# Kernel tuning notes

Hardware: AMD Instinct MI355X
Metric: run time of the kernel (lower is better)

Reference implementation:

```python
import jax, jax.numpy as jnp
import numpy as np

N_NODES = 50000
N_EDGES = 800000
IN_DIM = 128
H = 8
D = 16  # per-head out_dim; H*D == 128
CLAMP = 5.0


def setup_inputs() -> dict:
    key = jax.random.key(0)
    ks = jax.random.split(key, 9)
    xavier = lambda k, shape: jax.random.normal(k, shape, dtype=jnp.float32) * np.sqrt(2.0 / (shape[0] + shape[1]))
    x = jax.random.normal(ks[0], (N_NODES, IN_DIM), dtype=jnp.float32)
    edge_attr = jax.random.normal(ks[1], (N_EDGES, IN_DIM), dtype=jnp.float32)
    edge_index = jax.random.randint(ks[2], (2, N_EDGES), 0, N_NODES)
    WQ = xavier(ks[3], (IN_DIM, H * D))
    bQ = jnp.zeros((H * D,), dtype=jnp.float32)
    WK = xavier(ks[4], (IN_DIM, H * D))
    WV = xavier(ks[5], (IN_DIM, H * D))
    WE1 = xavier(ks[6], (IN_DIM, H * D))
    bE1 = jnp.zeros((H * D,), dtype=jnp.float32)
    return {"x": x, "edge_attr": edge_attr, "edge_index": edge_index,
            "WQ": WQ, "bQ": bQ, "WK": WK, "WV": WV, "WE1": WE1, "bE1": bE1}


def reference(x, edge_attr, edge_index, WQ, bQ, WK, WV, WE1, bE1):
    N = x.shape[0]
    src, dst = edge_index[0], edge_index[1]
    # projections (K/V have no bias: use_bias=False)
    Q = (x @ WQ + bQ).reshape(N, H, D)
    K = (x @ WK).reshape(N, H, D)
    V = (x @ WV).reshape(N, H, D)
    E = (edge_attr @ WE1 + bE1).reshape(-1, H, D)  # [Ne,H,D]
    # edge-gather elementwise QK product conditioned on E (attn_product='mul')
    score_e = K[src] * Q[dst] * E                  # [Ne,H,D]
    wE = score_e.reshape(score_e.shape[0], -1)     # [Ne,H*D]
    # scalar per-edge-per-head score (attn_reweight=False -> sum over D)
    score_h = score_e.sum(-1, keepdims=True) / jnp.sqrt(jnp.float32(D))
    score_h = jnp.clip(score_h, -CLAMP, CLAMP)     # [Ne,H,1]
    # pyg_softmax: segment-wise softmax keyed on destination node
    seg_max = jax.ops.segment_max(score_h, dst, num_segments=N)
    ex = jnp.exp(score_h - seg_max[dst])
    denom = jax.ops.segment_sum(ex, dst, num_segments=N)[dst] + 1e-16
    alpha = ex / denom                             # [Ne,H,1]
    # scatter-add aggregation of weighted values
    wV = jax.ops.segment_sum(V[src] * alpha, dst, num_segments=N)
    # edge enhance (edge_reweight=False -> rowV = score_e)
    wV = wV + jax.ops.segment_sum(score_e * alpha, dst, num_segments=N)
    return wV, wE
```

## Files before the change

kernel.cpp:

```cpp
#include <hip/hip_runtime.h>
#include <hip/hip_bf16.h>

#define NNODES 50000
#define NEDGES 800000
#define NHEAD 8

typedef __attribute__((ext_vector_type(8))) short short8v;
typedef __attribute__((ext_vector_type(4))) float f32x4;

union U8 { short8v v; unsigned short u[8]; };

__device__ inline unsigned short f2bf(float f) {
    unsigned int u = __float_as_uint(f);
    unsigned int r = (u + 0x7FFFu + ((u >> 16) & 1u)) >> 16;
    return (unsigned short)r;
}
__device__ inline float bf2f(unsigned int u) {
    return __uint_as_float(u << 16);
}

__global__ void prep_weights(const float* __restrict__ WQ, const float* __restrict__ WK,
                             const float* __restrict__ WV, const float* __restrict__ WE1,
                             unsigned short* __restrict__ Wt) {
    int idx = blockIdx.x * 256 + threadIdx.x;
    if (idx >= 4 * 16384) return;
    int m = idx >> 14, r = idx & 16383;
    int k = r >> 7, n = r & 127;
    const float* W = (m == 0) ? WQ : (m == 1) ? WK : (m == 2) ? WV : WE1;
    Wt[m * 16384 + n * 128 + k] = f2bf(W[k * 128 + n]);
}

__device__ inline int swz(int row, int byteInRow) {
    return row * 256 + (byteInRow ^ ((row & 15) << 4));
}

__device__ inline void stageW256(char* Wl, const unsigned short* __restrict__ Wtm, int t) {
    int row = t >> 1, half = t & 1;
    const unsigned short* src = Wtm + row * 128 + half * 64;
#pragma unroll
    for (int i = 0; i < 8; i++) {
        short8v v = *reinterpret_cast<const short8v*>(src + i * 8);
        *reinterpret_cast<short8v*>(Wl + swz(row, half * 128 + i * 16)) = v;
    }
}

__device__ inline void stageW512(char* Wl, const unsigned short* __restrict__ Wtm, int t) {
    int row = t >> 2, q = t & 3;
    const unsigned short* src = Wtm + row * 128 + q * 32;
#pragma unroll
    for (int i = 0; i < 4; i++) {
        short8v v = *reinterpret_cast<const short8v*>(src + i * 8);
        *reinterpret_cast<short8v*>(Wl + swz(row, q * 64 + i * 16)) = v;
    }
}

__device__ inline void loadAfrag(const float* aptr, int lg, short8v* a, bool ok) {
#pragma unroll
    for (int kk = 0; kk < 4; kk++) {
        U8 h;
        if (ok) {
            float4 f0 = *reinterpret_cast<const float4*>(aptr + kk * 32 + lg * 8);
            float4 f1 = *reinterpret_cast<const float4*>(aptr + kk * 32 + lg * 8 + 4);
            h.u[0] = f2bf(f0.x); h.u[1] = f2bf(f0.y); h.u[2] = f2bf(f0.z); h.u[3] = f2bf(f0.w);
            h.u[4] = f2bf(f1.x); h.u[5] = f2bf(f1.y); h.u[6] = f2bf(f1.z); h.u[7] = f2bf(f1.w);
        } else {
#pragma unroll
            for (int j = 0; j < 8; j++) h.u[j] = 0;
        }
        a[kk] = h.v;
    }
}

__global__ __launch_bounds__(256, 4) void proj_qkv(const float* __restrict__ x,
                                                   const unsigned short* __restrict__ Wt,
                                                   const float* __restrict__ bQ,
                                                   float* __restrict__ Q, float* __restrict__ K,
                                                   float* __restrict__ V) {
    __shared__ __align__(16) char Wl[32768];
    int t = threadIdx.x;
    int nb = blockIdx.x * 64;
    int lane = t & 63, w = t >> 6;
    int lg = lane >> 4, lr = lane & 15;

    int arow = nb + w * 16 + lr;
    bool ok = arow < NNODES;
    short8v a[4];
    loadAfrag(x + (size_t)arow * 128, lg, a, ok);

    float bq[8];
#pragma unroll
    for (int n = 0; n < 8; n++) bq[n] = bQ[n * 16 + lr];

    for (int m = 0; m < 3; m++) {
        __syncthreads();
        stageW256(Wl, Wt + m * 16384, t);
        __syncthreads();

        f32x4 acc[8];
#pragma unroll
        for (int n = 0; n < 8; n++) acc[n] = (f32x4){0.f, 0.f, 0.f, 0.f};
#pragma unroll
        for (int kk = 0; kk < 4; kk++) {
#pragma unroll
            for (int n = 0; n < 8; n++) {
                short8v b = *reinterpret_cast<short8v*>(Wl + swz(n * 16 + lr, (kk * 32 + lg * 8) * 2));
                acc[n] = __builtin_amdgcn_mfma_f32_16x16x32_bf16(a[kk], b, acc[n], 0, 0, 0);
            }
        }
        float* out = (m == 0) ? Q : (m == 1) ? K : V;
#pragma unroll
        for (int n = 0; n < 8; n++) {
            int c = n * 16 + lr;
            float bias = (m == 0) ? bq[n] : 0.f;
#pragma unroll
            for (int r = 0; r < 4; r++) {
                int gr = nb + w * 16 + lg * 4 + r;
                if (gr < NNODES) out[(size_t)gr * 128 + c] = acc[n][r] + bias;
            }
        }
    }
}

__global__ __launch_bounds__(512, 6) void edge_score(const float* __restrict__ EA,
                                                     const unsigned short* __restrict__ Wt,
                                                     const float* __restrict__ bE1,
                                                     const int* __restrict__ eidx,
                                                     const float* __restrict__ Q,
                                                     const float* __restrict__ K,
                                                     float* __restrict__ wE,
                                                     float* __restrict__ scoreH,
                                                     float* __restrict__ denom) {
    __shared__ __align__(16) char Wl[32768];
    __shared__ int srcL[128], dstL[128];
    int t = threadIdx.x;
    int eb = blockIdx.x * 128;
    int lane = t & 63, w = t >> 6;
    int lg = lane >> 4, lr = lane & 15;

    stageW512(Wl, Wt + 3 * 16384, t);
    if (t < 128) srcL[t] = eidx[eb + t];
    else if (t < 256) dstL[t - 128] = eidx[NEDGES + eb + t - 128];
    float be[8];
#pragma unroll
    for (int n = 0; n < 8; n++) be[n] = bE1[n * 16 + lr];

    int arow = eb + w * 16 + lr;
    short8v a[4];
    loadAfrag(EA + (size_t)arow * 128, lg, a, true);

    __syncthreads();

    f32x4 acc[8];
#pragma unroll
    for (int n = 0; n < 8; n++) acc[n] = (f32x4){0.f, 0.f, 0.f, 0.f};
#pragma unroll
    for (int kk = 0; kk < 4; kk++) {
#pragma unroll
        for (int n = 0; n < 8; n++) {
            short8v b = *reinterpret_cast<short8v*>(Wl + swz(n * 16 + lr, (kk * 32 + lg * 8) * 2));
            acc[n] = __builtin_amdgcn_mfma_f32_16x16x32_bf16(a[kk], b, acc[n], 0, 0, 0);
        }
    }

    __syncthreads();

#pragma unroll
    for (int n = 0; n < 8; n++) {
#pragma unroll
        for (int r = 0; r < 4; r++) {
            int row = w * 16 + lg * 4 + r;
            *reinterpret_cast<unsigned short*>(Wl + swz(row, (n * 16 + lr) * 2)) =
                f2bf(acc[n][r] + be[n]);
        }
    }

    int h = lane >> 3;
#pragma unroll 4
    for (int i = 0; i < 16; i++) {
        int loc = w * 16 + i;
        int e = eb + loc;
        int s = srcL[loc], d = dstL[loc];
        unsigned int ep = *reinterpret_cast<unsigned int*>(Wl + swz(loc, lane * 4));
        float e0 = bf2f(ep & 0xffffu);
        float e1 = bf2f(ep >> 16);
        float2 kv = *reinterpret_cast<const float2*>(K + (size_t)s * 128 + lane * 2);
        float2 qv = *reinterpret_cast<const float2*>(Q + (size_t)d * 128 + lane * 2);
        float s0 = e0 * kv.x * qv.x;
        float s1 = e1 * kv.y * qv.y;
        *reinterpret_cast<float2*>(wE + (size_t)e * 128 + lane * 2) = make_float2(s0, s1);
        float sum = s0 + s1;
        sum += __shfl_xor(sum, 1);
        sum += __shfl_xor(sum, 2);
        sum += __shfl_xor(sum, 4);
        if ((lane & 7) == 0) {
            float sh = fminf(fmaxf(sum * 0.25f, -5.f), 5.f);
            float ex = __expf(sh);
            scoreH[(size_t)e * 8 + h] = ex;
            unsafeAtomicAdd(&denom[d * 8 + h], ex);
        }
    }
}

__global__ void hist_kernel(const int* __restrict__ eidx, int* __restrict__ histo) {
    int e = blockIdx.x * 256 + threadIdx.x;
    if (e >= NEDGES) return;
    atomicAdd(&histo[eidx[NEDGES + e]], 1);
}

__global__ __launch_bounds__(256) void scanA(const int* __restrict__ histo, int* __restrict__ bsum) {
    __shared__ int l[4];
    int t = threadIdx.x;
    int idx = blockIdx.x * 256 + t;
    int v = (idx < NNODES) ? histo[idx] : 0;
#pragma unroll
    for (int off = 32; off; off >>= 1) v += __shfl_down(v, off);
    if ((t & 63) == 0) l[t >> 6] = v;
    __syncthreads();
    if (t == 0) bsum[blockIdx.x] = l[0] + l[1] + l[2] + l[3];
}

__global__ __launch_bounds__(256) void scanB(const int* __restrict__ bsum, int* __restrict__ boff) {
    __shared__ int l[256];
    int t = threadIdx.x;
    int v = (t < 196) ? bsum[t] : 0;
    l[t] = v;
    __syncthreads();
    for (int off = 1; off < 256; off <<= 1) {
        int tmp = (t >= off) ? l[t - off] : 0;
        __syncthreads();
        l[t] += tmp;
        __syncthreads();
    }
    if (t < 196) boff[t] = l[t] - v;
}

__global__ __launch_bounds__(256) void scanC(const int* __restrict__ histo,
                                             const int* __restrict__ boff,
                                             int* __restrict__ start, int* __restrict__ cursor) {
    __shared__ int l[256];
    int t = threadIdx.x;
    int idx = blockIdx.x * 256 + t;
    int v = (idx < NNODES) ? histo[idx] : 0;
    l[t] = v;
    __syncthreads();
    for (int off = 1; off < 256; off <<= 1) {
        int tmp = (t >= off) ? l[t - off] : 0;
        __syncthreads();
        l[t] += tmp;
        __syncthreads();
    }
    int excl = l[t] - v + boff[blockIdx.x];
    if (idx <= NNODES) {
        start[idx] = excl;
        if (idx < NNODES) cursor[idx] = excl;
    }
}

__global__ void scatter_edges(const int* __restrict__ eidx, int* __restrict__ cursor,
                              int* __restrict__ sortedE) {
    int e = blockIdx.x * 256 + threadIdx.x;
    if (e >= NEDGES) return;
    int d = eidx[NEDGES + e];
    int pos = atomicAdd(&cursor[d], 1);
    sortedE[pos] = e;
}

__global__ __launch_bounds__(256) void aggregate_pernode(const int* __restrict__ sortedE,
                                                         const int* __restrict__ start,
                                                         const int* __restrict__ eidx,
                                                         const float* __restrict__ scoreH,
                                                         const float* __restrict__ denom,
                                                         const float* __restrict__ V,
                                                         const float* __restrict__ wE,
                                                         float* __restrict__ wV) {
    __shared__ int eL[4][64];
    __shared__ int sL[4][64];
    __shared__ float aL[4][512];
    int w = threadIdx.x >> 6;
    int n = blockIdx.x * 4 + w;
    if (n >= NNODES) return;
    int lane = threadIdx.x & 63;
    int half = lane >> 5, li = lane & 31;
    int col = li * 4, h = li >> 2;
    int s0 = start[n], cnt = start[n + 1] - s0;

    float4 d0 = *reinterpret_cast<const float4*>(denom + n * 8);
    float4 d1 = *reinterpret_cast<const float4*>(denom + n * 8 + 4);
    float inv[8];
    inv[0] = 1.f / (d0.x + 1e-16f); inv[1] = 1.f / (d0.y + 1e-16f);
    inv[2] = 1.f / (d0.z + 1e-16f); inv[3] = 1.f / (d0.w + 1e-16f);
    inv[4] = 1.f / (d1.x + 1e-16f); inv[5] = 1.f / (d1.y + 1e-16f);
    inv[6] = 1.f / (d1.z + 1e-16f); inv[7] = 1.f / (d1.w + 1e-16f);

    float4 ac = make_float4(0.f, 0.f, 0.f, 0.f);

    for (int cb = 0; cb < cnt; cb += 64) {
        int ccnt = min(64, cnt - cb);
        int e = 0, s = 0;
        float4 p0 = make_float4(0.f, 0.f, 0.f, 0.f), p1 = p0;
        if (lane < ccnt) {
            e = sortedE[s0 + cb + lane];
            s = eidx[e];
            p0 = *reinterpret_cast<const float4*>(scoreH + (size_t)e * 8);
            p1 = *reinterpret_cast<const float4*>(scoreH + (size_t)e * 8 + 4);
        }
        eL[w][lane] = e;
        sL[w][lane] = s;
        aL[w][lane * 8 + 0] = p0.x * inv[0]; aL[w][lane * 8 + 1] = p0.y * inv[1];
        aL[w][lane * 8 + 2] = p0.z * inv[2]; aL[w][lane * 8 + 3] = p0.w * inv[3];
        aL[w][lane * 8 + 4] = p1.x * inv[4]; aL[w][lane * 8 + 5] = p1.y * inv[5];
        aL[w][lane * 8 + 6] = p1.z * inv[6]; aL[w][lane * 8 + 7] = p1.w * inv[7];
        asm volatile("s_waitcnt lgkmcnt(0)" ::: "memory");
        __builtin_amdgcn_sched_barrier(0);
        int np = (ccnt + 1) >> 1;
#pragma unroll 2
        for (int i = 0; i < np; i++) {
            int ii = i * 2 + half;
            int e2 = eL[w][ii], s2 = sL[w][ii];
            float al = aL[w][ii * 8 + h];
            float4 we = *reinterpret_cast<const float4*>(wE + (size_t)e2 * 128 + col);
            float4 vv = *reinterpret_cast<const float4*>(V + (size_t)s2 * 128 + col);
            ac.x += (vv.x + we.x) * al;
            ac.y += (vv.y + we.y) * al;
            ac.z += (vv.z + we.z) * al;
            ac.w += (vv.w + we.w) * al;
        }
    }
    ac.x += __shfl_xor(ac.x, 32);
    ac.y += __shfl_xor(ac.y, 32);
    ac.z += __shfl_xor(ac.z, 32);
    ac.w += __shfl_xor(ac.w, 32);
    if (half == 0) *reinterpret_cast<float4*>(wV + (size_t)n * 128 + col) = ac;
}

extern "C" void kernel_launch(void* const* d_in, const int* in_sizes, int n_in,
                              void* d_out, int out_size, void* d_ws, size_t ws_size,
                              hipStream_t stream) {
    const float* x    = (const float*)d_in[0];
    const float* ea   = (const float*)d_in[1];
    const int*   eidx = (const int*)d_in[2];
    const float* WQ   = (const float*)d_in[3];
    const float* bQ   = (const float*)d_in[4];
    const float* WK   = (const float*)d_in[5];
    const float* WV   = (const float*)d_in[6];
    const float* WE1  = (const float*)d_in[7];
    const float* bE1  = (const float*)d_in[8];

    float* wV = (float*)d_out;
    float* wE = (float*)d_out + (size_t)NNODES * 128;

    float* Q      = (float*)d_ws;
    float* K      = Q + (size_t)NNODES * 128;
    float* V      = K + (size_t)NNODES * 128;
    float* scoreH = V + (size_t)NNODES * 128;
    float* denom  = scoreH + (size_t)NEDGES * 8;
    unsigned short* Wt = (unsigned short*)(denom + (size_t)NNODES * 8);
    int* histo   = (int*)(Wt + 4 * 16384);
    int* start   = histo + 50176;
    int* cursor  = start + 50177;
    int* sortedE = cursor + 50176;
    int* bsum    = sortedE + NEDGES;
    int* boff    = bsum + 256;

    hipMemsetAsync(histo, 0, (size_t)50176 * 4, stream);
    hipMemsetAsync(denom, 0, (size_t)NNODES * 8 * 4, stream);

    prep_weights<<<(4 * 16384 + 255) / 256, 256, 0, stream>>>(WQ, WK, WV, WE1, Wt);
    hist_kernel<<<(NEDGES + 255) / 256, 256, 0, stream>>>(eidx, histo);
    scanA<<<196, 256, 0, stream>>>(histo, bsum);
    scanB<<<1, 256, 0, stream>>>(bsum, boff);
    scanC<<<196, 256, 0, stream>>>(histo, boff, start, cursor);
    scatter_edges<<<(NEDGES + 255) / 256, 256, 0, stream>>>(eidx, cursor, sortedE);
    proj_qkv<<<(NNODES + 63) / 64, 256, 0, stream>>>(x, Wt, bQ, Q, K, V);
    edge_score<<<NEDGES / 128, 512, 0, stream>>>(ea, Wt, bE1, eidx, Q, K, wE, scoreH, denom);
    aggregate_pernode<<<(NNODES + 3) / 4, 256, 0, stream>>>(sortedE, start, eidx, scoreH, denom, V, wE, wV);
}
```

Baseline: 536.7 us.

## Fuse edge scoring and per-node aggregation into one destination-partitioned kernel

```diff
diff --git a/kernel.cpp b/kernel.cpp
--- a/kernel.cpp
+++ b/kernel.cpp
@@ -4,6 +4,9 @@
 #define NNODES 50000
 #define NEDGES 800000
 #define NHEAD 8
+#define CAP 96
+#define NBLK ((NEDGES + CAP - 1) / CAP)
+#define MAXSPAN 384
 
 typedef __attribute__((ext_vector_type(8))) short short8v;
 typedef __attribute__((ext_vector_type(4))) float f32x4;
@@ -121,86 +124,6 @@
     }
 }
 
-__global__ __launch_bounds__(512, 6) void edge_score(const float* __restrict__ EA,
-                                                     const unsigned short* __restrict__ Wt,
-                                                     const float* __restrict__ bE1,
-                                                     const int* __restrict__ eidx,
-                                                     const float* __restrict__ Q,
-                                                     const float* __restrict__ K,
-                                                     float* __restrict__ wE,
-                                                     float* __restrict__ scoreH,
-                                                     float* __restrict__ denom) {
-    __shared__ __align__(16) char Wl[32768];
-    __shared__ int srcL[128], dstL[128];
-    int t = threadIdx.x;
-    int eb = blockIdx.x * 128;
-    int lane = t & 63, w = t >> 6;
-    int lg = lane >> 4, lr = lane & 15;
-
-    stageW512(Wl, Wt + 3 * 16384, t);
-    if (t < 128) srcL[t] = eidx[eb + t];
-    else if (t < 256) dstL[t - 128] = eidx[NEDGES + eb + t - 128];
-    float be[8];
-#pragma unroll
-    for (int n = 0; n < 8; n++) be[n] = bE1[n * 16 + lr];
-
-    int arow = eb + w * 16 + lr;
-    short8v a[4];
-    loadAfrag(EA + (size_t)arow * 128, lg, a, true);
-
-    __syncthreads();
-
-    f32x4 acc[8];
-#pragma unroll
-    for (int n = 0; n < 8; n++) acc[n] = (f32x4){0.f, 0.f, 0.f, 0.f};
-#pragma unroll
-    for (int kk = 0; kk < 4; kk++) {
-#pragma unroll
-        for (int n = 0; n < 8; n++) {
-            short8v b = *reinterpret_cast<short8v*>(Wl + swz(n * 16 + lr, (kk * 32 + lg * 8) * 2));
-            acc[n] = __builtin_amdgcn_mfma_f32_16x16x32_bf16(a[kk], b, acc[n], 0, 0, 0);
-        }
-    }
-
-    __syncthreads();
-
-#pragma unroll
-    for (int n = 0; n < 8; n++) {
-#pragma unroll
-        for (int r = 0; r < 4; r++) {
-            int row = w * 16 + lg * 4 + r;
-            *reinterpret_cast<unsigned short*>(Wl + swz(row, (n * 16 + lr) * 2)) =
-                f2bf(acc[n][r] + be[n]);
-        }
-    }
-
-    int h = lane >> 3;
-#pragma unroll 4
-    for (int i = 0; i < 16; i++) {
-        int loc = w * 16 + i;
-        int e = eb + loc;
-        int s = srcL[loc], d = dstL[loc];
-        unsigned int ep = *reinterpret_cast<unsigned int*>(Wl + swz(loc, lane * 4));
-        float e0 = bf2f(ep & 0xffffu);
-        float e1 = bf2f(ep >> 16);
-        float2 kv = *reinterpret_cast<const float2*>(K + (size_t)s * 128 + lane * 2);
-        float2 qv = *reinterpret_cast<const float2*>(Q + (size_t)d * 128 + lane * 2);
-        float s0 = e0 * kv.x * qv.x;
-        float s1 = e1 * kv.y * qv.y;
-        *reinterpret_cast<float2*>(wE + (size_t)e * 128 + lane * 2) = make_float2(s0, s1);
-        float sum = s0 + s1;
-        sum += __shfl_xor(sum, 1);
-        sum += __shfl_xor(sum, 2);
-        sum += __shfl_xor(sum, 4);
-        if ((lane & 7) == 0) {
-            float sh = fminf(fmaxf(sum * 0.25f, -5.f), 5.f);
-            float ex = __expf(sh);
-            scoreH[(size_t)e * 8 + h] = ex;
-            unsafeAtomicAdd(&denom[d * 8 + h], ex);
-        }
-    }
-}
-
 __global__ void hist_kernel(const int* __restrict__ eidx, int* __restrict__ histo) {
     int e = blockIdx.x * 256 + threadIdx.x;
     if (e >= NEDGES) return;
@@ -265,59 +188,132 @@
     sortedE[pos] = e;
 }
 
-__global__ __launch_bounds__(256) void aggregate_pernode(const int* __restrict__ sortedE,
-                                                         const int* __restrict__ start,
-                                                         const int* __restrict__ eidx,
-                                                         const float* __restrict__ scoreH,
-                                                         const float* __restrict__ denom,
-                                                         const float* __restrict__ V,
-                                                         const float* __restrict__ wE,
-                                                         float* __restrict__ wV) {
-    __shared__ int eL[4][64];
-    __shared__ int sL[4][64];
-    __shared__ float aL[4][512];
-    int w = threadIdx.x >> 6;
-    int n = blockIdx.x * 4 + w;
-    if (n >= NNODES) return;
-    int lane = threadIdx.x & 63;
+__global__ void partition_blocks(const int* __restrict__ start, int* __restrict__ firstNode) {
+    int b = blockIdx.x * 256 + threadIdx.x;
+    if (b > NBLK) return;
+    int target = b * CAP;
+    int lo = 0, hi = NNODES;
+    while (lo < hi) {
+        int mid = (lo + hi) >> 1;
+        if (start[mid] < target) lo = mid + 1; else hi = mid;
+    }
+    firstNode[b] = lo;
+}
+
+__global__ __launch_bounds__(512, 6) void edge_mega(const float* __restrict__ EA,
+                                                    const unsigned short* __restrict__ Wt,
+                                                    const float* __restrict__ bE1,
+                                                    const int* __restrict__ eidx,
+                                                    const float* __restrict__ Q,
+                                                    const float* __restrict__ K,
+                                                    const float* __restrict__ V,
+                                                    const int* __restrict__ sortedE,
+                                                    const int* __restrict__ start,
+                                                    const int* __restrict__ firstNode,
+                                                    float* __restrict__ wE,
+                                                    float* __restrict__ wV) {
+    __shared__ __align__(16) char Wl[32768];
+    __shared__ float exL[MAXSPAN][8];
+    __shared__ int eG[MAXSPAN], sG[MAXSPAN], dG[MAXSPAN];
+
+    int b = blockIdx.x;
+    int n0 = firstNode[b], n1 = firstNode[b + 1];
+    if (n0 >= n1) return;
+    int gbase = start[n0];
+    int span = start[n1] - gbase;
+    if (span > MAXSPAN) span = MAXSPAN;
+
+    int t = threadIdx.x;
+    int lane = t & 63, w = t >> 6;
+    int lg = lane >> 4, lr = lane & 15;
+
+    for (int i = t; i < span; i += 512) {
+        int e = sortedE[gbase + i];
+        eG[i] = e;
+        sG[i] = eidx[e];
+        dG[i] = eidx[NEDGES + e];
+    }
+    __syncthreads();
+
+    float be[8];
+#pragma unroll
+    for (int n = 0; n < 8; n++) be[n] = bE1[n * 16 + lr];
+
+    for (int base = 0; base < span; base += 128) {
+        stageW512(Wl, Wt + 3 * 16384, t);
+
+        int slot = base + w * 16 + lr;
+        bool act = slot < span;
+        short8v a[4];
+        loadAfrag(EA + (size_t)(act ? eG[slot] : 0) * 128, lg, a, act);
+
+        __syncthreads();
+
+        f32x4 acc[8];
+#pragma unroll
+        for (int n = 0; n < 8; n++) acc[n] = (f32x4){0.f, 0.f, 0.f, 0.f};
+#pragma unroll
+        for (int kk = 0; kk < 4; kk++) {
+#pragma unroll
+            for (int n = 0; n < 8; n++) {
+                short8v bfr = *reinterpret_cast<short8v*>(Wl + swz(n * 16 + lr, (kk * 32 + lg * 8) * 2));
+                acc[n] = __builtin_amdgcn_mfma_f32_16x16x32_bf16(a[kk], bfr, acc[n], 0, 0, 0);
+            }
+        }
+        __syncthreads();
+
+#pragma unroll
+        for (int n = 0; n < 8; n++) {
+#pragma unroll
+            for (int r = 0; r < 4; r++) {
+                int row = w * 16 + lg * 4 + r;
+                *reinterpret_cast<unsigned short*>(Wl + swz(row, (n * 16 + lr) * 2)) =
+                    f2bf(acc[n][r] + be[n]);
+            }
+        }
+        int h = lane >> 3;
+#pragma unroll 4
+        for (int i = 0; i < 16; i++) {
+            int loc = w * 16 + i;
+            int slot2 = base + loc;
+            if (slot2 >= span) break;
+            int e = eG[slot2], s = sG[slot2], d = dG[slot2];
+            unsigned int ep = *reinterpret_cast<unsigned int*>(Wl + swz(loc, lane * 4));
+            float e0 = bf2f(ep & 0xffffu);
+            float e1 = bf2f(ep >> 16);
+            float2 kv = *reinterpret_cast<const float2*>(K + (size_t)s * 128 + lane * 2);
+            float2 qv = *reinterpret_cast<const float2*>(Q + (size_t)d * 128 + lane * 2);
+            float s0 = e0 * kv.x * qv.x;
+            float s1 = e1 * kv.y * qv.y;
+            *reinterpret_cast<float2*>(wE + (size_t)e * 128 + lane * 2) = make_float2(s0, s1);
+            float sum = s0 + s1;
+            sum += __shfl_xor(sum, 1);
+            sum += __shfl_xor(sum, 2);
+            sum += __shfl_xor(sum, 4);
+            if ((lane & 7) == 0) {
+                float sh = fminf(fmaxf(sum * 0.25f, -5.f), 5.f);
+                exL[slot2][h] = __expf(sh);
+            }
+        }
+        __syncthreads();
+    }
+
     int half = lane >> 5, li = lane & 31;
-    int col = li * 4, h = li >> 2;
-    int s0 = start[n], cnt = start[n + 1] - s0;
-
-    float4 d0 = *reinterpret_cast<const float4*>(denom + n * 8);
-    float4 d1 = *reinterpret_cast<const float4*>(denom + n * 8 + 4);
-    float inv[8];
-    inv[0] = 1.f / (d0.x + 1e-16f); inv[1] = 1.f / (d0.y + 1e-16f);
-    inv[2] = 1.f / (d0.z + 1e-16f); inv[3] = 1.f / (d0.w + 1e-16f);
-    inv[4] = 1.f / (d1.x + 1e-16f); inv[5] = 1.f / (d1.y + 1e-16f);
-    inv[6] = 1.f / (d1.z + 1e-16f); inv[7] = 1.f / (d1.w + 1e-16f);
-
-    float4 ac = make_float4(0.f, 0.f, 0.f, 0.f);
-
-    for (int cb = 0; cb < cnt; cb += 64) {
-        int ccnt = min(64, cnt - cb);
-        int e = 0, s = 0;
-        float4 p0 = make_float4(0.f, 0.f, 0.f, 0.f), p1 = p0;
-        if (lane < ccnt) {
-            e = sortedE[s0 + cb + lane];
-            s = eidx[e];
-            p0 = *reinterpret_cast<const float4*>(scoreH + (size_t)e * 8);
-            p1 = *reinterpret_cast<const float4*>(scoreH + (size_t)e * 8 + 4);
-        }
-        eL[w][lane] = e;
-        sL[w][lane] = s;
-        aL[w][lane * 8 + 0] = p0.x * inv[0]; aL[w][lane * 8 + 1] = p0.y * inv[1];
-        aL[w][lane * 8 + 2] = p0.z * inv[2]; aL[w][lane * 8 + 3] = p0.w * inv[3];
-        aL[w][lane * 8 + 4] = p1.x * inv[4]; aL[w][lane * 8 + 5] = p1.y * inv[5];
-        aL[w][lane * 8 + 6] = p1.z * inv[6]; aL[w][lane * 8 + 7] = p1.w * inv[7];
-        asm volatile("s_waitcnt lgkmcnt(0)" ::: "memory");
-        __builtin_amdgcn_sched_barrier(0);
-        int np = (ccnt + 1) >> 1;
-#pragma unroll 2
-        for (int i = 0; i < np; i++) {
-            int ii = i * 2 + half;
-            int e2 = eL[w][ii], s2 = sL[w][ii];
-            float al = aL[w][ii * 8 + h];
+    int col = li * 4, h2 = li >> 2;
+    int hh = lane >> 3, j = lane & 7;
+    for (int n = n0 + w; n < n1; n += 8) {
+        int sl0 = start[n] - gbase, sl1 = start[n + 1] - gbase;
+        float den = 0.f;
+        for (int ss = sl0 + j; ss < sl1; ss += 8) den += exL[ss][hh];
+        den += __shfl_xor(den, 1);
+        den += __shfl_xor(den, 2);
+        den += __shfl_xor(den, 4);
+        float inv = 1.f / (den + 1e-16f);
+        float alinv = __shfl(inv, h2 * 8);
+        float4 ac = make_float4(0.f, 0.f, 0.f, 0.f);
+        for (int ss = sl0 + half; ss < sl1; ss += 2) {
+            int e2 = eG[ss], s2 = sG[ss];
+            float al = exL[ss][h2] * alinv;
             float4 we = *reinterpret_cast<const float4*>(wE + (size_t)e2 * 128 + col);
             float4 vv = *reinterpret_cast<const float4*>(V + (size_t)s2 * 128 + col);
             ac.x += (vv.x + we.x) * al;
@@ -325,12 +321,12 @@
             ac.z += (vv.z + we.z) * al;
             ac.w += (vv.w + we.w) * al;
         }
-    }
-    ac.x += __shfl_xor(ac.x, 32);
-    ac.y += __shfl_xor(ac.y, 32);
-    ac.z += __shfl_xor(ac.z, 32);
-    ac.w += __shfl_xor(ac.w, 32);
-    if (half == 0) *reinterpret_cast<float4*>(wV + (size_t)n * 128 + col) = ac;
+        ac.x += __shfl_xor(ac.x, 32);
+        ac.y += __shfl_xor(ac.y, 32);
+        ac.z += __shfl_xor(ac.z, 32);
+        ac.w += __shfl_xor(ac.w, 32);
+        if (half == 0) *reinterpret_cast<float4*>(wV + (size_t)n * 128 + col) = ac;
+    }
 }
 
 extern "C" void kernel_launch(void* const* d_in, const int* in_sizes, int n_in,
@@ -352,18 +348,16 @@
     float* Q      = (float*)d_ws;
     float* K      = Q + (size_t)NNODES * 128;
     float* V      = K + (size_t)NNODES * 128;
-    float* scoreH = V + (size_t)NNODES * 128;
-    float* denom  = scoreH + (size_t)NEDGES * 8;
-    unsigned short* Wt = (unsigned short*)(denom + (size_t)NNODES * 8);
-    int* histo   = (int*)(Wt + 4 * 16384);
-    int* start   = histo + 50176;
-    int* cursor  = start + 50177;
-    int* sortedE = cursor + 50176;
-    int* bsum    = sortedE + NEDGES;
-    int* boff    = bsum + 256;
+    unsigned short* Wt = (unsigned short*)(V + (size_t)NNODES * 128);
+    int* histo     = (int*)(Wt + 4 * 16384);
+    int* start     = histo + 50176;
+    int* cursor    = start + 50177;
+    int* sortedE   = cursor + 50176;
+    int* bsum      = sortedE + NEDGES;
+    int* boff      = bsum + 256;
+    int* firstNode = boff + 256;
 
     hipMemsetAsync(histo, 0, (size_t)50176 * 4, stream);
-    hipMemsetAsync(denom, 0, (size_t)NNODES * 8 * 4, stream);
 
     prep_weights<<<(4 * 16384 + 255) / 256, 256, 0, stream>>>(WQ, WK, WV, WE1, Wt);
     hist_kernel<<<(NEDGES + 255) / 256, 256, 0, stream>>>(eidx, histo);
@@ -371,7 +365,8 @@
     scanB<<<1, 256, 0, stream>>>(bsum, boff);
     scanC<<<196, 256, 0, stream>>>(histo, boff, start, cursor);
     scatter_edges<<<(NEDGES + 255) / 256, 256, 0, stream>>>(eidx, cursor, sortedE);
+    partition_blocks<<<(NBLK + 256) / 256, 256, 0, stream>>>(start, firstNode);
     proj_qkv<<<(NNODES + 63) / 64, 256, 0, stream>>>(x, Wt, bQ, Q, K, V);
-    edge_score<<<NEDGES / 128, 512, 0, stream>>>(ea, Wt, bE1, eidx, Q, K, wE, scoreH, denom);
-    aggregate_pernode<<<(NNODES + 3) / 4, 256, 0, stream>>>(sortedE, start, eidx, scoreH, denom, V, wE, wV);
-}
+    edge_mega<<<NBLK, 512, 0, stream>>>(ea, Wt, bE1, eidx, Q, K, V, sortedE, start,
+                                        firstNode, wE, wV);
+}
```

Result: slower. 879.4 us (+63.9%).
